# Optimization experiments

Hardware: AMD Instinct MI355X
Metric: run time of the kernel (lower is better)

The kernel has to match this reference:

```python
import jax, jax.numpy as jnp
import numpy as np

# Instant-NGP style multi-level hash encoding constants (match init_kwargs)
N_LEVELS = 16
N_ENC = 16384          # per-level hashmap size (power of two)
N_EMBED = 2
MIN_RES = 16
MAX_RES = 512
HIDDEN = 64
P1 = np.uint32(2654435761)  # spatial hash primes (Instant-NGP)
P2 = np.uint32(805459861)


def _resolutions():
    b = np.exp((np.log(MAX_RES) - np.log(MIN_RES)) / (N_LEVELS - 1))
    return [int(np.floor(MIN_RES * b ** l)) for l in range(N_LEVELS)]


def _hash_encode(x, tables):
    """x: (B,3) in [-1,1]; tables: (L, T, E). Returns (B, L*E)."""
    feats = []
    for l, res in enumerate(_resolutions()):
        xg = (x + 1.0) * (0.5 * (res - 1))          # map [-1,1] -> [0, res-1]
        x0f = jnp.floor(xg)
        w = xg - x0f                                # (B,3) trilinear weights
        i0 = jnp.clip(x0f.astype(jnp.int32), 0, res - 1)
        i1 = jnp.clip(i0 + 1, 0, res - 1)
        dense = (res ** 3) <= N_ENC                 # small levels index densely
        feat = jnp.zeros((x.shape[0], N_EMBED), dtype=x.dtype)
        for cz in (0, 1):
            for cy in (0, 1):
                for cx in (0, 1):
                    ix = i1[:, 0] if cx else i0[:, 0]
                    iy = i1[:, 1] if cy else i0[:, 1]
                    iz = i1[:, 2] if cz else i0[:, 2]
                    if dense:
                        idx = ix + res * (iy + res * iz)
                    else:
                        idx = (ix.astype(jnp.uint32)
                               ^ (iy.astype(jnp.uint32) * P1)
                               ^ (iz.astype(jnp.uint32) * P2)) & np.uint32(N_ENC - 1)
                        idx = idx.astype(jnp.int32)
                    wc = ((w[:, 0] if cx else 1.0 - w[:, 0])
                          * (w[:, 1] if cy else 1.0 - w[:, 1])
                          * (w[:, 2] if cz else 1.0 - w[:, 2]))
                    feat = feat + wc[:, None] * tables[l, idx]
        feats.append(feat)
    return jnp.concatenate(feats, axis=-1)          # (B, 32)


def setup_inputs() -> dict:
    key = jax.random.key(0)
    ks = jax.random.split(key, 10)
    B = 1048576
    x = jax.random.uniform(ks[0], (B, 3), minval=-1.0, maxval=1.0)
    tables = jax.random.uniform(ks[1], (N_LEVELS, N_ENC, N_EMBED),
                                minval=-1e-4, maxval=1e-4)

    def lin(k, fin, fout):
        s = 1.0 / np.sqrt(fin)
        kw, kb = jax.random.split(k)
        return (jax.random.uniform(kw, (fin, fout), minval=-s, maxval=s),
                jax.random.uniform(kb, (fout,), minval=-s, maxval=s))

    w1, b1 = lin(ks[2], N_LEVELS * N_EMBED, HIDDEN)
    w2, b2 = lin(ks[3], HIDDEN, HIDDEN)
    w3, b3 = lin(ks[4], HIDDEN, 16)
    cw1, cb1 = lin(ks[5], 16, HIDDEN)
    cw2, cb2 = lin(ks[6], HIDDEN, HIDDEN)
    cw3, cb3 = lin(ks[7], HIDDEN, HIDDEN)
    cw4, cb4 = lin(ks[8], HIDDEN, 3)
    return {"x": x, "tables": tables,
            "w1": w1, "b1": b1, "w2": w2, "b2": b2, "w3": w3, "b3": b3,
            "cw1": cw1, "cb1": cb1, "cw2": cw2, "cb2": cb2,
            "cw3": cw3, "cb3": cb3, "cw4": cw4, "cb4": cb4}


def reference(x, tables, w1, b1, w2, b2, w3, b3,
              cw1, cb1, cw2, cb2, cw3, cb3, cw4, cb4):
    h = _hash_encode(x, tables)                     # (B, 32)
    d = jax.nn.relu(h @ w1 + b1)
    d = jax.nn.relu(d @ w2 + b2)
    d = d @ w3 + b3                                 # (B, 16)
    c = jax.nn.relu(d @ cw1 + cb1)
    c = jax.nn.relu(c @ cw2 + cb2)
    c = jax.nn.relu(c @ cw3 + cb3)
    c = jax.nn.sigmoid(c @ cw4 + cb4)               # is_hdr=False -> sigmoid
    sigma = jnp.exp(d[:, 0])                        # (B,)
    return sigma, c
```

## Files before the change

kernel.cpp:

```cpp
#include <hip/hip_runtime.h>

typedef __bf16 bf8 __attribute__((ext_vector_type(8)));
typedef float f4 __attribute__((ext_vector_type(4)));
typedef unsigned short us4 __attribute__((ext_vector_type(4)));
typedef unsigned int u32x4 __attribute__((ext_vector_type(4)));

#define MFMA16(a,b,c) __builtin_amdgcn_mfma_f32_16x16x32_bf16((a),(b),(c),0,0,0)

#define BLOCK 512
#define NWAVE 8

__device__ __forceinline__ unsigned short f2bfu(float f){
  __bf16 h = (__bf16)f;
  union { __bf16 b; unsigned short u; } v; v.b = h; return v.u;
}
__device__ __forceinline__ float ubfu(unsigned int u16){
  union { unsigned int i; float f; } v; v.i = u16 << 16; return v.f;
}

__device__ __forceinline__ void wfence(){
  asm volatile("s_waitcnt lgkmcnt(0)" ::: "memory");
}

#define OFF_W1   0
#define OFF_W2   2048
#define OFF_W3   6144
#define OFF_CW1  7168
#define OFF_CW2  8192
#define OFF_CW3  12288
#define OFF_CW4  16384
#define OFF_ACT  17408
#define ACT_STRIDE 72
#define SMEM_US  (17408 + NWAVE*16*ACT_STRIDE)

#define BO_B1  0
#define BO_B2  64
#define BO_B3  128
#define BO_CB1 144
#define BO_CB2 208
#define BO_CB3 272
#define BO_CB4 336

template<int FIN,int FOUT,int KS,int MT>
__device__ __forceinline__ void stage_w(const float* w, unsigned short* dst){
  const int total = KS*MT*512;
  for (int e = threadIdx.x; e < total; e += BLOCK){
    int chunk = e >> 9;
    int s = chunk / MT, t = chunk % MT;
    int le = e & 511;
    int lane = le >> 3, j = le & 7;
    int q = lane >> 4, m = lane & 15;
    int i = s*32 + q*8 + j;
    int o = t*16 + m;
    dst[e] = (i < FIN && o < FOUT) ? f2bfu(w[i*FOUT + o]) : (unsigned short)0;
  }
}

__device__ __forceinline__ void stage_cw1(const float* w, unsigned short* dst){
  for (int e = threadIdx.x; e < 1024; e += BLOCK){
    int t = e >> 8;
    int le = e & 255;
    int lane = le >> 3, j = e & 7;
    int q = lane >> 4, m = lane & 15;
    dst[e] = f2bfu(w[(q*8+j)*64 + t*16 + m]);
  }
}

__device__ __forceinline__ void layer64(const unsigned short* wlds, const unsigned short* bias,
                                        unsigned short* act, int lane, bool relu){
  const int q = lane >> 4, m = lane & 15;
  bf8 b0 = *(const bf8*)(act + m*ACT_STRIDE + q*8);
  bf8 b1 = *(const bf8*)(act + m*ACT_STRIDE + 32 + q*8);
  f4 acc[4];
#pragma unroll
  for (int t = 0; t < 4; ++t){
    f4 c = {0.f,0.f,0.f,0.f};
    c = MFMA16(*(const bf8*)(wlds + ((0*4+t)*64+lane)*8), b0, c);
    c = MFMA16(*(const bf8*)(wlds + ((1*4+t)*64+lane)*8), b1, c);
    acc[t] = c;
  }
#pragma unroll
  for (int t = 0; t < 4; ++t){
    us4 bb = *(const us4*)(bias + t*16 + q*4);
    us4 pk;
#pragma unroll
    for (int r = 0; r < 4; ++r){
      float v = acc[t][r] + ubfu(bb[r]);
      if (relu) v = fmaxf(v, 0.f);
      pk[r] = f2bfu(v);
    }
    *(us4*)(act + m*ACT_STRIDE + t*16 + q*4) = pk;
  }
}

#define STAGE_ALL_WEIGHTS()                                                  \
  stage_w<32,64,1,4>(w1,  smem+OFF_W1);                                      \
  stage_w<64,64,2,4>(w2,  smem+OFF_W2);                                      \
  stage_w<64,16,2,1>(w3,  smem+OFF_W3);                                      \
  stage_cw1(cw1, smem+OFF_CW1);                                              \
  stage_w<64,64,2,4>(cw2, smem+OFF_CW2);                                     \
  stage_w<64,64,2,4>(cw3, smem+OFF_CW3);                                     \
  stage_w<64, 3,2,1>(cw4, smem+OFF_CW4);                                     \
  {                                                                          \
    int t = threadIdx.x;                                                     \
    if (t < 64){                                                             \
      sbias[BO_B1 +t] = f2bfu(b1[t]);                                        \
      sbias[BO_B2 +t] = f2bfu(b2[t]);                                        \
      sbias[BO_CB1+t] = f2bfu(cb1[t]);                                       \
      sbias[BO_CB2+t] = f2bfu(cb2[t]);                                       \
      sbias[BO_CB3+t] = f2bfu(cb3[t]);                                       \
    }                                                                        \
    if (t < 16) sbias[BO_B3+t] = f2bfu(b3[t]);                               \
    if (t < 3)  sbias[BO_CB4+t] = f2bfu(cb4[t]);                             \
  }

#define MLP_BODY(bfrag, gp)                                                  \
    {                                                                        \
      f4 acc[4];                                                             \
      _Pragma("unroll")                                                      \
      for (int t = 0; t < 4; ++t){                                           \
        f4 c = {0.f,0.f,0.f,0.f};                                            \
        acc[t] = MFMA16(*(const bf8*)(smem + OFF_W1 + (t*64+lane)*8), bfrag, c);\
      }                                                                      \
      _Pragma("unroll")                                                      \
      for (int t = 0; t < 4; ++t){                                           \
        us4 bb = *(const us4*)(sbias + BO_B1 + t*16 + q*4);                  \
        us4 pk;                                                              \
        _Pragma("unroll")                                                    \
        for (int r = 0; r < 4; ++r){                                         \
          float v = fmaxf(acc[t][r] + ubfu(bb[r]), 0.f);                     \
          pk[r] = f2bfu(v);                                                  \
        }                                                                    \
        *(us4*)(act + m*ACT_STRIDE + t*16 + q*4) = pk;                       \
      }                                                                      \
    }                                                                        \
    wfence();                                                                \
    layer64(smem+OFF_W2, sbias+BO_B2, act, lane, true);                      \
    wfence();                                                                \
    {                                                                        \
      bf8 b0 = *(const bf8*)(act + m*ACT_STRIDE + q*8);                      \
      bf8 b1 = *(const bf8*)(act + m*ACT_STRIDE + 32 + q*8);                 \
      f4 c = {0.f,0.f,0.f,0.f};                                              \
      c = MFMA16(*(const bf8*)(smem + OFF_W3 + lane*8), b0, c);              \
      c = MFMA16(*(const bf8*)(smem + OFF_W3 + (64+lane)*8), b1, c);         \
      us4 bb = *(const us4*)(sbias + BO_B3 + q*4);                           \
      us4 pk;                                                                \
      float d0 = 0.f;                                                        \
      _Pragma("unroll")                                                      \
      for (int r = 0; r < 4; ++r){                                           \
        float v = c[r] + ubfu(bb[r]);                                        \
        if (r == 0) d0 = v;                                                  \
        pk[r] = f2bfu(v);                                                    \
      }                                                                      \
      if (q == 0 && gp < nB) out[gp] = expf(d0);                             \
      *(us4*)(act + m*ACT_STRIDE + q*4) = pk;                                \
    }                                                                        \
    wfence();                                                                \
    {                                                                        \
      bf8 bc, aw[4];                                                         \
      if (q < 2){                                                            \
        bc = *(const bf8*)(act + m*ACT_STRIDE + q*8);                        \
        _Pragma("unroll")                                                    \
        for (int t = 0; t < 4; ++t)                                          \
          aw[t] = *(const bf8*)(smem + OFF_CW1 + (t*32+lane)*8);             \
      } else {                                                               \
        _Pragma("unroll")                                                    \
        for (int j = 0; j < 8; ++j) bc[j] = (__bf16)0.f;                     \
        _Pragma("unroll")                                                    \
        for (int t = 0; t < 4; ++t) aw[t] = bc;                              \
      }                                                                      \
      f4 acc[4];                                                             \
      _Pragma("unroll")                                                      \
      for (int t = 0; t < 4; ++t){                                           \
        f4 c = {0.f,0.f,0.f,0.f};                                            \
        acc[t] = MFMA16(aw[t], bc, c);                                       \
      }                                                                      \
      _Pragma("unroll")                                                      \
      for (int t = 0; t < 4; ++t){                                           \
        us4 bb = *(const us4*)(sbias + BO_CB1 + t*16 + q*4);                 \
        us4 pk;                                                              \
        _Pragma("unroll")                                                    \
        for (int r = 0; r < 4; ++r){                                         \
          float v = fmaxf(acc[t][r] + ubfu(bb[r]), 0.f);                     \
          pk[r] = f2bfu(v);                                                  \
        }                                                                    \
        *(us4*)(act + m*ACT_STRIDE + t*16 + q*4) = pk;                       \
      }                                                                      \
    }                                                                        \
    wfence();                                                                \
    layer64(smem+OFF_CW2, sbias+BO_CB2, act, lane, true);                    \
    wfence();                                                                \
    layer64(smem+OFF_CW3, sbias+BO_CB3, act, lane, true);                    \
    wfence();                                                                \
    {                                                                        \
      bf8 b0 = *(const bf8*)(act + m*ACT_STRIDE + q*8);                      \
      bf8 b1 = *(const bf8*)(act + m*ACT_STRIDE + 32 + q*8);                 \
      f4 c = {0.f,0.f,0.f,0.f};                                              \
      c = MFMA16(*(const bf8*)(smem + OFF_CW4 + lane*8), b0, c);             \
      c = MFMA16(*(const bf8*)(smem + OFF_CW4 + (64+lane)*8), b1, c);        \
      if (q == 0 && gp < nB){                                                \
        _Pragma("unroll")                                                    \
        for (int r = 0; r < 3; ++r){                                         \
          float v = c[r] + ubfu(sbias[BO_CB4 + r]);                          \
          out[nB + gp*3 + r] = 1.f/(1.f + expf(-v));                         \
        }                                                                    \
      }                                                                      \
    }                                                                        \
    wfence();

#define CH 16384
__global__ __launch_bounds__(512) void hash_phase(
    const float* __restrict__ xin, const float* __restrict__ tab,
    unsigned int* __restrict__ feat, int nB)
{
  __shared__ unsigned int stab[16384];
  __shared__ int sres[16];
  const int lvl = blockIdx.y;
  {
    const float2* t2 = (const float2*)tab + (lvl<<14);
    for (int e = threadIdx.x; e < 16384; e += 512){
      float2 v = t2[e];
      stab[e] = ((unsigned)f2bfu(v.y) << 16) | (unsigned)f2bfu(v.x);
    }
    if (threadIdx.x < 16){
      const int R[16] = {16,20,25,32,40,50,64,80,101,128,161,203,256,322,406,512};
      sres[threadIdx.x] = R[threadIdx.x];
    }
  }
  __syncthreads();

  const int res = sres[lvl];
  const float sc = 0.5f*(float)(res-1);
  const bool dense = (lvl < 3);
  unsigned int* fout = feat + (size_t)lvl * (size_t)nB;

  int pend = (blockIdx.x + 1) * CH; if (pend > nB) pend = nB;
  for (int p = blockIdx.x*CH + threadIdx.x; p < pend; p += 512){
    const float px = xin[p*3+0], py = xin[p*3+1], pz = xin[p*3+2];
    const float xs=(px+1.f)*sc, ys=(py+1.f)*sc, zs=(pz+1.f)*sc;
    const float fx=floorf(xs), fy=floorf(ys), fz=floorf(zs);
    const float wx=xs-fx, wy=ys-fy, wz=zs-fz;
    int ix0=min(max((int)fx,0),res-1);
    int iy0=min(max((int)fy,0),res-1);
    int iz0=min(max((int)fz,0),res-1);
    int ix1=min(ix0+1,res-1), iy1=min(iy0+1,res-1), iz1=min(iz0+1,res-1);
    unsigned X0,X1,Y0,Y1,Z0,Z1;
    if (dense){
      X0=(unsigned)ix0;            X1=(unsigned)ix1;
      Y0=(unsigned)(res*iy0);      Y1=(unsigned)(res*iy1);
      Z0=(unsigned)(res*res*iz0);  Z1=(unsigned)(res*res*iz1);
    } else {
      X0=(unsigned)ix0;                 X1=(unsigned)ix1;
      Y0=(unsigned)iy0*2654435761u;     Y1=(unsigned)iy1*2654435761u;
      Z0=(unsigned)iz0*805459861u;      Z1=(unsigned)iz1*805459861u;
    }
    const float wx0=1.f-wx, wy0=1.f-wy, wz0=1.f-wz;
    float f0=0.f, f1=0.f;
#pragma unroll
    for (int c = 0; c < 8; ++c){
      unsigned xc = (c&1)?X1:X0;
      unsigned yc = (c&2)?Y1:Y0;
      unsigned zc = (c&4)?Z1:Z0;
      unsigned idx = dense ? (xc+yc+zc) : ((xc^yc^zc)&16383u);
      unsigned tv = stab[idx];
      float wc = ((c&1)?wx:wx0) * ((c&2)?wy:wy0) * ((c&4)?wz:wz0);
      f0 += wc*ubfu(tv << 16);
      f1 += wc*ubfu(tv & 0xffff0000u);
    }
    fout[p] = ((unsigned)f2bfu(f1) << 16) | (unsigned)f2bfu(f0);
  }
}

__global__ __launch_bounds__(BLOCK) void mlp_phase(
    const unsigned int* __restrict__ feat,
    const float* __restrict__ w1,  const float* __restrict__ b1,
    const float* __restrict__ w2,  const float* __restrict__ b2,
    const float* __restrict__ w3,  const float* __restrict__ b3,
    const float* __restrict__ cw1, const float* __restrict__ cb1,
    const float* __restrict__ cw2, const float* __restrict__ cb2,
    const float* __restrict__ cw3, const float* __restrict__ cb3,
    const float* __restrict__ cw4, const float* __restrict__ cb4,
    float* __restrict__ out, int nB)
{
  __shared__ __align__(16) unsigned short smem[SMEM_US];
  __shared__ __align__(16) unsigned short sbias[344];
  STAGE_ALL_WEIGHTS();
  __syncthreads();

  const int lane = threadIdx.x & 63, wv = threadIdx.x >> 6;
  const int q = lane >> 4, m = lane & 15;
  unsigned short* act = smem + OFF_ACT + wv*16*ACT_STRIDE;
  const unsigned int* fq = feat + (size_t)(4*q) * (size_t)nB;

  for (int it = 0; it < 4; ++it){
    const int gp  = blockIdx.x*BLOCK + wv*64 + it*16 + m;
    const int gpl = min(gp, nB-1);
    union { u32x4 u; bf8 b; } fb;
    fb.u[0] = fq[gpl];
    fb.u[1] = fq[(size_t)nB   + gpl];
    fb.u[2] = fq[(size_t)nB*2 + gpl];
    fb.u[3] = fq[(size_t)nB*3 + gpl];
    bf8 bfrag = fb.b;
    MLP_BODY(bfrag, gp)
  }
}

__global__ __launch_bounds__(BLOCK) void nerf_fused(
    const float* __restrict__ xin, const float* __restrict__ tab,
    const float* __restrict__ w1,  const float* __restrict__ b1,
    const float* __restrict__ w2,  const float* __restrict__ b2,
    const float* __restrict__ w3,  const float* __restrict__ b3,
    const float* __restrict__ cw1, const float* __restrict__ cb1,
    const float* __restrict__ cw2, const float* __restrict__ cb2,
    const float* __restrict__ cw3, const float* __restrict__ cb3,
    const float* __restrict__ cw4, const float* __restrict__ cb4,
    float* __restrict__ out, int nB)
{
  __shared__ __align__(16) unsigned short smem[SMEM_US];
  __shared__ __align__(16) unsigned short sbias[344];
  __shared__ int sres[16];
  STAGE_ALL_WEIGHTS();
  if (threadIdx.x < 16){
    const int R[16] = {16,20,25,32,40,50,64,80,101,128,161,203,256,322,406,512};
    sres[threadIdx.x] = R[threadIdx.x];
  }
  __syncthreads();

  const int lane = threadIdx.x & 63, wv = threadIdx.x >> 6;
  const int q = lane >> 4, m = lane & 15;
  unsigned short* act = smem + OFF_ACT + wv*16*ACT_STRIDE;

  int res_[4];
#pragma unroll
  for (int d = 0; d < 4; ++d) res_[d] = sres[4*q + d];

  for (int it = 0; it < 4; ++it){
    const int gp  = blockIdx.x*BLOCK + wv*64 + it*16 + m;
    const int gpl = min(gp, nB-1);
    const float px = xin[gpl*3+0];
    const float py = xin[gpl*3+1];
    const float pz = xin[gpl*3+2];

    bf8 bfrag;
#pragma unroll
    for (int d = 0; d < 4; ++d){
      const int lvl = 4*q + d;
      const int res = res_[d];
      const float sc = 0.5f*(float)(res-1);
      const float xs=(px+1.f)*sc, ys=(py+1.f)*sc, zs=(pz+1.f)*sc;
      const float fx=floorf(xs), fy=floorf(ys), fz=floorf(zs);
      const float wx=xs-fx, wy=ys-fy, wz=zs-fz;
      int ix0=min(max((int)fx,0),res-1);
      int iy0=min(max((int)fy,0),res-1);
      int iz0=min(max((int)fz,0),res-1);
      int ix1=min(ix0+1,res-1), iy1=min(iy0+1,res-1), iz1=min(iz0+1,res-1);
      const bool dense = (lvl < 3);
      unsigned X0,X1,Y0,Y1,Z0,Z1;
      if (dense){
        X0=(unsigned)ix0;            X1=(unsigned)ix1;
        Y0=(unsigned)(res*iy0);      Y1=(unsigned)(res*iy1);
        Z0=(unsigned)(res*res*iz0);  Z1=(unsigned)(res*res*iz1);
      } else {
        X0=(unsigned)ix0;                 X1=(unsigned)ix1;
        Y0=(unsigned)iy0*2654435761u;     Y1=(unsigned)iy1*2654435761u;
        Z0=(unsigned)iz0*805459861u;      Z1=(unsigned)iz1*805459861u;
      }
      const float wx0=1.f-wx, wy0=1.f-wy, wz0=1.f-wz;
      float f0=0.f, f1=0.f;
      const float2* tl = (const float2*)tab + (lvl<<14);
#pragma unroll
      for (int c = 0; c < 8; ++c){
        unsigned xc = (c&1)?X1:X0;
        unsigned yc = (c&2)?Y1:Y0;
        unsigned zc = (c&4)?Z1:Z0;
        unsigned idx = dense ? (xc+yc+zc) : ((xc^yc^zc)&16383u);
        float2 tv = tl[idx];
        float wc = ((c&1)?wx:wx0) * ((c&2)?wy:wy0) * ((c&4)?wz:wz0);
        f0 += wc*tv.x;
        f1 += wc*tv.y;
      }
      bfrag[2*d]   = (__bf16)f0;
      bfrag[2*d+1] = (__bf16)f1;
    }
    MLP_BODY(bfrag, gp)
  }
}

extern "C" void kernel_launch(void* const* d_in, const int* in_sizes, int n_in,
                              void* d_out, int out_size, void* d_ws, size_t ws_size,
                              hipStream_t stream) {
  (void)n_in; (void)out_size;
  const int nB = in_sizes[0] / 3;
  const float* xin = (const float*)d_in[0];
  const float* tab = (const float*)d_in[1];
  const float *w1=(const float*)d_in[2],  *b1=(const float*)d_in[3];
  const float *w2=(const float*)d_in[4],  *b2=(const float*)d_in[5];
  const float *w3=(const float*)d_in[6],  *b3=(const float*)d_in[7];
  const float *cw1=(const float*)d_in[8], *cb1=(const float*)d_in[9];
  const float *cw2=(const float*)d_in[10],*cb2=(const float*)d_in[11];
  const float *cw3=(const float*)d_in[12],*cb3=(const float*)d_in[13];
  const float *cw4=(const float*)d_in[14],*cb4=(const float*)d_in[15];
  float* out = (float*)d_out;

  const size_t need = (size_t)nB * 16u * 4u;
  if (ws_size >= need){
    dim3 ga((nB + CH - 1) / CH, 16);
    hash_phase<<<ga, dim3(512), 0, stream>>>(xin, tab, (unsigned int*)d_ws, nB);
    const int blocks = (nB + BLOCK - 1) / BLOCK;
    mlp_phase<<<dim3(blocks), dim3(BLOCK), 0, stream>>>(
        (const unsigned int*)d_ws, w1,b1,w2,b2,w3,b3,
        cw1,cb1,cw2,cb2,cw3,cb3,cw4,cb4, out, nB);
  } else {
    const int blocks = (nB + BLOCK - 1) / BLOCK;
    nerf_fused<<<dim3(blocks), dim3(BLOCK), 0, stream>>>(
        xin, tab, w1,b1,w2,b2,w3,b3,
        cw1,cb1,cw2,cb2,cw3,cb3,cw4,cb4, out, nB);
  }
}
```

Baseline: 198.3 us.

## Rewrite MLP phase with 32x32 MFMA and register-resident activations

Replaces the 16x16 MFMA MLP kernel with one using 32x32x16 bf16 MFMA. Activations are transposed between layers in registers via permlane32 swaps instead of round-tripping through shared memory. Each block now handles 1024 points with the next iteration's features prefetched, and launch bounds request 3 blocks per CU. This is meant to cut LDS traffic and MFMA issue count, at the cost of higher register pressure and padded weight tiles for the narrow layers.

```diff
diff --git a/kernel.cpp b/kernel.cpp
--- a/kernel.cpp
+++ b/kernel.cpp
@@ -2,10 +2,12 @@
 
 typedef __bf16 bf8 __attribute__((ext_vector_type(8)));
 typedef float f4 __attribute__((ext_vector_type(4)));
+typedef float f32x16 __attribute__((ext_vector_type(16)));
 typedef unsigned short us4 __attribute__((ext_vector_type(4)));
 typedef unsigned int u32x4 __attribute__((ext_vector_type(4)));
 
 #define MFMA16(a,b,c) __builtin_amdgcn_mfma_f32_16x16x32_bf16((a),(b),(c),0,0,0)
+#define MFMA32(a,b,c) __builtin_amdgcn_mfma_f32_32x32x16_bf16((a),(b),(c),0,0,0)
 
 #define BLOCK 512
 #define NWAVE 8
@@ -271,7 +273,99 @@
   }
 }
 
-__global__ __launch_bounds__(BLOCK) void mlp_phase(
+
+#define W32_W1   0
+#define W32_W2   2048
+#define W32_W3   6144
+#define W32_CW1  8192
+#define W32_CW2  9216
+#define W32_CW3  13312
+#define W32_CW4  17408
+#define W32_TOT  19456
+
+#define SB_B1  0
+#define SB_B2  64
+#define SB_CB1 128
+#define SB_CB2 192
+#define SB_CB3 256
+#define SB_B3  320
+#define SB_CB4 352
+
+template<int FIN,int FOUT,int MT,int KT>
+__device__ __forceinline__ void stage32(const float* w, unsigned short* dst){
+  const int total = MT*KT*512;
+  for (int e = threadIdx.x; e < total; e += BLOCK){
+    int frag = e >> 9;
+    int mt = frag / KT, kt = frag % KT;
+    int l  = (e >> 3) & 63, j = e & 7;
+    int i  = kt*16 + ((l >> 5) << 3) + j;
+    int o  = mt*32 + (l & 31);
+    dst[e] = (i < FIN && o < FOUT) ? f2bfu(w[i*FOUT + o]) : (unsigned short)0;
+  }
+}
+
+__device__ __forceinline__ unsigned pk2(float x, float y){
+  typedef __bf16 bf2v __attribute__((ext_vector_type(2)));
+  union { bf2v b; unsigned u; } v;
+  v.b[0] = (__bf16)x; v.b[1] = (__bf16)y;
+  return v.u;
+}
+
+__device__ __forceinline__ bf8 mkbf8(unsigned d0, unsigned d1, unsigned d2, unsigned d3){
+  union { u32x4 u; bf8 b; } v;
+  v.u[0] = d0; v.u[1] = d1; v.u[2] = d2; v.u[3] = d3;
+  return v.b;
+}
+
+__device__ __forceinline__ void swap_half(unsigned a, unsigned b, unsigned& x, unsigned& y){
+#if __has_builtin(__builtin_amdgcn_permlane32_swap)
+  auto r = __builtin_amdgcn_permlane32_swap(a, b, false, false);
+  x = r[0]; y = r[1];
+#else
+  unsigned sa = (unsigned)__shfl_xor((int)a, 32, 64);
+  unsigned sb = (unsigned)__shfl_xor((int)b, 32, 64);
+  bool lo = (threadIdx.x & 32) == 0;
+  x = lo ? a : sb;
+  y = lo ? sa : b;
+#endif
+}
+
+__device__ __forceinline__ f32x16 bias16(const float* sb, int h4){
+  f4 c0 = *(const f4*)(sb + h4);
+  f4 c1 = *(const f4*)(sb + 8  + h4);
+  f4 c2 = *(const f4*)(sb + 16 + h4);
+  f4 c3 = *(const f4*)(sb + 24 + h4);
+  f32x16 c;
+#pragma unroll
+  for (int r = 0; r < 4; ++r){
+    c[r] = c0[r]; c[4+r] = c1[r]; c[8+r] = c2[r]; c[12+r] = c3[r];
+  }
+  return c;
+}
+
+__device__ __forceinline__ void trans2(const f32x16 a0, const f32x16 a1, bf8* B){
+  unsigned p0[8], p1[8];
+#pragma unroll
+  for (int p = 0; p < 8; ++p){
+    p0[p] = pk2(fmaxf(a0[2*p], 0.f), fmaxf(a0[2*p+1], 0.f));
+    p1[p] = pk2(fmaxf(a1[2*p], 0.f), fmaxf(a1[2*p+1], 0.f));
+  }
+#pragma unroll
+  for (int o = 0; o < 2; ++o){
+    unsigned x0,y0,x1,y1;
+    swap_half(p0[4*o+0], p0[4*o+2], x0, y0);
+    swap_half(p0[4*o+1], p0[4*o+3], x1, y1);
+    B[o] = mkbf8(x0, x1, y0, y1);
+    swap_half(p1[4*o+0], p1[4*o+2], x0, y0);
+    swap_half(p1[4*o+1], p1[4*o+3], x1, y1);
+    B[2+o] = mkbf8(x0, x1, y0, y1);
+  }
+}
+
+#define PTS_PER_BLOCK 1024
+#define M_ITERS 4
+
+__global__ __launch_bounds__(BLOCK, 3) void mlp32_phase(
     const unsigned int* __restrict__ feat,
     const float* __restrict__ w1,  const float* __restrict__ b1,
     const float* __restrict__ w2,  const float* __restrict__ b2,
@@ -282,27 +376,123 @@
     const float* __restrict__ cw4, const float* __restrict__ cb4,
     float* __restrict__ out, int nB)
 {
-  __shared__ __align__(16) unsigned short smem[SMEM_US];
-  __shared__ __align__(16) unsigned short sbias[344];
-  STAGE_ALL_WEIGHTS();
+  __shared__ __align__(16) unsigned short sw[W32_TOT];
+  __shared__ __align__(16) float sbf[384];
+  stage32<32,64,2,2>(w1,  sw+W32_W1);
+  stage32<64,64,2,4>(w2,  sw+W32_W2);
+  stage32<64,16,1,4>(w3,  sw+W32_W3);
+  stage32<16,64,2,1>(cw1, sw+W32_CW1);
+  stage32<64,64,2,4>(cw2, sw+W32_CW2);
+  stage32<64,64,2,4>(cw3, sw+W32_CW3);
+  stage32<64, 3,1,4>(cw4, sw+W32_CW4);
+  {
+    int t = threadIdx.x;
+    if (t < 64){
+      sbf[SB_B1 +t] = b1[t];
+      sbf[SB_B2 +t] = b2[t];
+      sbf[SB_CB1+t] = cb1[t];
+      sbf[SB_CB2+t] = cb2[t];
+      sbf[SB_CB3+t] = cb3[t];
+    }
+    if (t >= 64 && t < 96)  sbf[SB_B3  + t-64] = (t-64 < 16) ? b3[t-64]  : 0.f;
+    if (t >= 96 && t < 128) sbf[SB_CB4 + t-96] = (t-96 < 3)  ? cb4[t-96] : 0.f;
+  }
   __syncthreads();
 
-  const int lane = threadIdx.x & 63, wv = threadIdx.x >> 6;
-  const int q = lane >> 4, m = lane & 15;
-  unsigned short* act = smem + OFF_ACT + wv*16*ACT_STRIDE;
-  const unsigned int* fq = feat + (size_t)(4*q) * (size_t)nB;
-
-  for (int it = 0; it < 4; ++it){
-    const int gp  = blockIdx.x*BLOCK + wv*64 + it*16 + m;
-    const int gpl = min(gp, nB-1);
-    union { u32x4 u; bf8 b; } fb;
-    fb.u[0] = fq[gpl];
-    fb.u[1] = fq[(size_t)nB   + gpl];
-    fb.u[2] = fq[(size_t)nB*2 + gpl];
-    fb.u[3] = fq[(size_t)nB*3 + gpl];
-    bf8 bfrag = fb.b;
-    MLP_BODY(bfrag, gp)
-  }
+  const int l  = threadIdx.x & 63, wv = threadIdx.x >> 6;
+  const int h  = l >> 5, n = l & 31, h4 = h << 2;
+  const int base0 = blockIdx.x * PTS_PER_BLOCK + wv*32 + n;
+
+#define FR(off, frag) (*(const bf8*)(sw + (off) + ((frag) << 9) + (l << 3)))
+#define LOADF(d0, d1, g) {                                                   \
+    int gg = min((g), nB-1);                                                 \
+    _Pragma("unroll")                                                        \
+    for (int d = 0; d < 4; ++d){                                             \
+      d0[d] = feat[(size_t)(h4 + d)*(size_t)nB + gg];                        \
+      d1[d] = feat[(size_t)(8 + h4 + d)*(size_t)nB + gg];                    \
+    } }
+
+  u32x4 f0, f1, nf0, nf1;
+  LOADF(f0, f1, base0)
+
+  for (int it = 0; it < M_ITERS; ++it){
+    const int gp = base0 + it*256;
+    bf8 B[4];
+    B[0] = mkbf8(f0[0], f0[1], f0[2], f0[3]);
+    B[1] = mkbf8(f1[0], f1[1], f1[2], f1[3]);
+
+    f32x16 a0 = bias16(sbf + SB_B1,      h4);
+    f32x16 a1 = bias16(sbf + SB_B1 + 32, h4);
+    a0 = MFMA32(FR(W32_W1,0), B[0], a0);
+    a0 = MFMA32(FR(W32_W1,1), B[1], a0);
+    a1 = MFMA32(FR(W32_W1,2), B[0], a1);
+    a1 = MFMA32(FR(W32_W1,3), B[1], a1);
+
+    if (it + 1 < M_ITERS){ LOADF(nf0, nf1, gp + 256) }
+
+    trans2(a0, a1, B);
+
+    a0 = bias16(sbf + SB_B2,      h4);
+    a1 = bias16(sbf + SB_B2 + 32, h4);
+#pragma unroll
+    for (int kt = 0; kt < 4; ++kt){
+      a0 = MFMA32(FR(W32_W2, kt),   B[kt], a0);
+      a1 = MFMA32(FR(W32_W2, 4+kt), B[kt], a1);
+    }
+    trans2(a0, a1, B);
+
+    f32x16 ad = bias16(sbf + SB_B3, h4);
+#pragma unroll
+    for (int kt = 0; kt < 4; ++kt) ad = MFMA32(FR(W32_W3, kt), B[kt], ad);
+    if (h == 0 && gp < nB) out[gp] = expf(ad[0]);
+    {
+      unsigned q0 = pk2(ad[0], ad[1]);
+      unsigned q1 = pk2(ad[2], ad[3]);
+      unsigned q2 = pk2(ad[4], ad[5]);
+      unsigned q3 = pk2(ad[6], ad[7]);
+      unsigned x0,y0,x1,y1;
+      swap_half(q0, q2, x0, y0);
+      swap_half(q1, q3, x1, y1);
+      B[0] = mkbf8(x0, x1, y0, y1);
+    }
+
+    a0 = bias16(sbf + SB_CB1,      h4);
+    a1 = bias16(sbf + SB_CB1 + 32, h4);
+    a0 = MFMA32(FR(W32_CW1,0), B[0], a0);
+    a1 = MFMA32(FR(W32_CW1,1), B[0], a1);
+    trans2(a0, a1, B);
+
+    a0 = bias16(sbf + SB_CB2,      h4);
+    a1 = bias16(sbf + SB_CB2 + 32, h4);
+#pragma unroll
+    for (int kt = 0; kt < 4; ++kt){
+      a0 = MFMA32(FR(W32_CW2, kt),   B[kt], a0);
+      a1 = MFMA32(FR(W32_CW2, 4+kt), B[kt], a1);
+    }
+    trans2(a0, a1, B);
+
+    a0 = bias16(sbf + SB_CB3,      h4);
+    a1 = bias16(sbf + SB_CB3 + 32, h4);
+#pragma unroll
+    for (int kt = 0; kt < 4; ++kt){
+      a0 = MFMA32(FR(W32_CW3, kt),   B[kt], a0);
+      a1 = MFMA32(FR(W32_CW3, 4+kt), B[kt], a1);
+    }
+    trans2(a0, a1, B);
+
+    f32x16 ac = bias16(sbf + SB_CB4, h4);
+#pragma unroll
+    for (int kt = 0; kt < 4; ++kt) ac = MFMA32(FR(W32_CW4, kt), B[kt], ac);
+    if (h == 0 && gp < nB){
+      out[nB + gp*3 + 0] = 1.f/(1.f + expf(-ac[0]));
+      out[nB + gp*3 + 1] = 1.f/(1.f + expf(-ac[1]));
+      out[nB + gp*3 + 2] = 1.f/(1.f + expf(-ac[2]));
+    }
+
+    if (it + 1 < M_ITERS){ f0 = nf0; f1 = nf1; }
+  }
+#undef FR
+#undef LOADF
 }
 
 __global__ __launch_bounds__(BLOCK) void nerf_fused(
@@ -406,8 +596,8 @@
   if (ws_size >= need){
     dim3 ga((nB + CH - 1) / CH, 16);
     hash_phase<<<ga, dim3(512), 0, stream>>>(xin, tab, (unsigned int*)d_ws, nB);
-    const int blocks = (nB + BLOCK - 1) / BLOCK;
-    mlp_phase<<<dim3(blocks), dim3(BLOCK), 0, stream>>>(
+    const int blocks = (nB + PTS_PER_BLOCK - 1) / PTS_PER_BLOCK;
+    mlp32_phase<<<dim3(blocks), dim3(BLOCK), 0, stream>>>(
         (const unsigned int*)d_ws, w1,b1,w2,b2,w3,b3,
         cw1,cb1,cw2,cb2,cw3,cb3,cw4,cb4, out, nB);
   } else {
```

New measurement: 605.1 us. +205.1%, slower.
